# Kernel optimization log

Hardware: AMD Instinct MI355X
Metric: run time of the kernel (lower is better)

The kernel has to match this reference:

```python
import jax, jax.numpy as jnp
import numpy as np

B, T, D, C = 16, 2048, 512, 20
K_EASY, K_HARD = 40, 20
M_BIG, M_SMALL = 7, 3
A4 = A5 = A6 = A7 = 1.0
EPS = 1e-05
DROP_P = 0.6


def setup_inputs() -> dict:
    key = jax.random.key(0)
    ks = jax.random.split(key, 6)
    attn = jax.random.uniform(ks[0], (B, T, 1), dtype=jnp.float32)
    mu = jax.random.normal(ks[1], (B, T, D), dtype=jnp.float32)
    var = jax.random.uniform(ks[2], (B, T, D), dtype=jnp.float32) * 0.9 + 0.1
    mu_clip = jax.random.normal(ks[3], (B, T, D), dtype=jnp.float32)
    text_feat = jax.random.normal(ks[4], (C, D), dtype=jnp.float32)
    keep = (jax.random.uniform(ks[5], (B, T)) >= DROP_P).astype(jnp.float32)
    drop_mask = keep / (1.0 - DROP_P)  # inverted-dropout mask on a ones tensor
    return dict(attn=attn, mu=mu, var=var, mu_clip=mu_clip, text_feat=text_feat, drop_mask=drop_mask)


def _normalize(x, axis=-1):
    n = jnp.linalg.norm(x, axis=axis, keepdims=True)
    return x / jnp.maximum(n, 1e-12)


def _select_topk(scores, emb, k):
    # torch: sort desc, take first k indices, gather along time dim
    _, idx = jax.lax.top_k(scores, k)  # [B,k]
    return jnp.take_along_axis(emb, idx[:, :, None], axis=1)  # [B,k,D]


def _window_reduce(x, w, op_min):
    # binary erosion/dilation along time with structure ones((1,w)), border_value=0
    lo, hi = w // 2, w - 1 - w // 2
    xp = jnp.pad(x, ((0, 0), (lo, hi)), constant_values=0.0)
    if op_min:
        return jax.lax.reduce_window(xp, jnp.inf, jax.lax.min, (1, w), (1, 1), 'VALID')
    return jax.lax.reduce_window(xp, -jnp.inf, jax.lax.max, (1, w), (1, 1), 'VALID')


def _kl_distance(mu_p, cov_p, mu_q, cov_q):
    # vectorized over all (i in k_p) x (j in k_q) pairs
    cov_p = cov_p + EPS
    cov_q = cov_q + EPS
    d = mu_p.shape[-1]
    diff = mu_q[:, None, :, :] - mu_p[:, :, None, :]        # [B,kp,kq,D]
    term1 = 0.5 * jnp.sum(diff * diff / cov_q[:, None, :, :], axis=-1)
    term2 = 0.5 * (jnp.sum(jnp.log(cov_q), -1)[:, None, :] - jnp.sum(jnp.log(cov_p), -1)[:, :, None])
    term3 = 0.5 * jnp.sum(cov_p[:, :, None, :] / cov_q[:, None, :, :], axis=-1)
    dist = term1 + term2 + term3 - 0.5 * d
    return jnp.mean(1.0 / (dist + 1.0), axis=(1, 2))        # [B]


def _prob_contrastive(hard_q, easy_pos, easy_neg):
    pos = _kl_distance(hard_q[0], hard_q[1], easy_pos[0], easy_pos[1])
    neg = _kl_distance(hard_q[0], hard_q[1], easy_neg[0], easy_neg[1])
    return jnp.mean(-(jnp.log(pos) + jnp.log(1.0 - neg)))


def _forward(attn, mu, var, mu_clip, text_feat, drop_mask):
    a = attn[..., 0]                                        # [B,T]
    a_drop = a * drop_mask
    a_rev = jnp.max(a, axis=1, keepdims=True) - a
    a_rev_drop = a_rev * drop_mask
    easy_act = (_select_topk(a_drop, mu, K_EASY), _select_topk(a_drop, var, K_EASY))
    easy_bkg = (_select_topk(a_rev_drop, mu, K_EASY), _select_topk(a_rev_drop, var, K_EASY))

    med = jnp.median(a, axis=1, keepdims=True)
    abin = jnp.where(a > med, 1.0, 0.0)
    er_M = _window_reduce(abin, M_BIG, True)
    er_m = _window_reduce(abin, M_SMALL, True)
    inner = jax.lax.stop_gradient(er_m - er_M)              # mask computed on detached numpy in torch
    dl_m = _window_reduce(abin, M_SMALL, False)
    dl_M = _window_reduce(abin, M_BIG, False)
    outer = jax.lax.stop_gradient(dl_M - dl_m)
    a_inner = a * inner
    a_outer = a * outer
    hard_act = (_select_topk(a_inner, mu, K_HARD), _select_topk(a_inner, var, K_HARD))
    hard_bkg = (_select_topk(a_outer, mu, K_HARD), _select_topk(a_outer, var, K_HARD))

    # Distillation
    sim = jnp.einsum('btd,btd->bt', _normalize(mu), _normalize(mu_clip))
    distill = A4 * (-jnp.log(jnp.mean((sim + 1.0) / 2.0)))

    act_loss = A5 * _prob_contrastive(hard_act, easy_act, easy_bkg)
    bkg_loss = A6 * _prob_contrastive(hard_bkg, easy_bkg, easy_act)

    emb = _normalize(text_feat)
    sim_m = emb @ jax.lax.stop_gradient(emb.T) - jnp.eye(emb.shape[0], dtype=emb.dtype)
    ortho = A7 * jnp.linalg.norm(sim_m)

    total = distill + act_loss + bkg_loss + ortho
    return total, distill, act_loss, bkg_loss, ortho


def reference(attn, mu, var, mu_clip, text_feat, drop_mask):
    return _forward(attn, mu, var, mu_clip, text_feat, drop_mask)
```

## Files before the change

### kernel.cpp

```cpp
#include <hip/hip_runtime.h>
#include <math.h>


#define BB 16
#define TT 2048
#define DD 512
#define CC 20
#define KEASY 40
#define KHARD 20
#define EPSF 1e-5f

typedef unsigned long long u64;

template <int CTRL>
__device__ __forceinline__ float dpp_mov(float x) {
  return __int_as_float(__builtin_amdgcn_update_dpp(
      0, __float_as_int(x), CTRL, 0xF, 0xF, true));
}
__device__ __forceinline__ float wsum63(float v) {
  v += dpp_mov<0x111>(v);
  v += dpp_mov<0x112>(v);
  v += dpp_mov<0x114>(v);
  v += dpp_mov<0x118>(v);
  v += dpp_mov<0x142>(v);
  v += dpp_mov<0x143>(v);
  return v;
}
__device__ __forceinline__ float wsum_bc(float v) {
  return __int_as_float(__builtin_amdgcn_readlane(__float_as_int(wsum63(v)), 63));
}
__device__ __forceinline__ float wmax_bc(float v) {
  v = fmaxf(v, dpp_mov<0x111>(v));
  v = fmaxf(v, dpp_mov<0x112>(v));
  v = fmaxf(v, dpp_mov<0x114>(v));
  v = fmaxf(v, dpp_mov<0x118>(v));
  v = fmaxf(v, dpp_mov<0x142>(v));
  v = fmaxf(v, dpp_mov<0x143>(v));
  return __int_as_float(__builtin_amdgcn_readlane(__float_as_int(v), 63));
}

__device__ __forceinline__ float kth_val(const float (&v)[32], unsigned k, unsigned hi) {
  unsigned lo = 0;
  while (lo < hi) {
    const unsigned mid = lo + ((hi - lo + 1) >> 1);
    const float mf = __uint_as_float(mid);
    unsigned c = 0;
#pragma unroll
    for (int r = 0; r < 32; r++) c += (unsigned)__popcll(__ballot(v[r] >= mf));
    if (c >= k) lo = mid; else hi = mid - 1;
  }
  return __uint_as_float(lo);
}

__global__ __launch_bounds__(256, 1) void k_main1(const float* __restrict__ attn,
                                                  const float* __restrict__ drop,
                                                  const float* __restrict__ mu,
                                                  const float* __restrict__ muc,
                                                  const float* __restrict__ var,
                                                  int* __restrict__ idxb,
                                                  float* __restrict__ slogb,
                                                  float* __restrict__ part,
                                                  double* __restrict__ acc) {
  const int tid = threadIdx.x, wid = tid >> 6, lane = tid & 63;

  if (blockIdx.x >= 64) {
    __shared__ float s_red[4];
    const int blk = blockIdx.x - 64;
    const float* pmu = mu + (size_t)(blk * 4 + wid) * DD + lane * 4;
    const float* pmc = muc + (size_t)(blk * 4 + wid) * DD + lane * 4;
    float4 xa = *(const float4*)(pmu);
    float4 xb = *(const float4*)(pmu + 256);
    float4 ya = *(const float4*)(pmc);
    float4 yb = *(const float4*)(pmc + 256);
    float wacc = 0.f;
#pragma unroll
    for (int it = 0; it < 4; it++) {
      const float4 cxa = xa, cxb = xb, cya = ya, cyb = yb;
      if (it < 3) {
        const size_t off = (size_t)(it + 1) * 8192 * DD;
        xa = *(const float4*)(pmu + off);
        xb = *(const float4*)(pmu + off + 256);
        ya = *(const float4*)(pmc + off);
        yb = *(const float4*)(pmc + off + 256);
      }
      float dot = 0.f, n1 = 0.f, n2 = 0.f;
      dot = fmaf(cxa.x, cya.x, fmaf(cxa.y, cya.y, fmaf(cxa.z, cya.z, fmaf(cxa.w, cya.w, dot))));
      n1 = fmaf(cxa.x, cxa.x, fmaf(cxa.y, cxa.y, fmaf(cxa.z, cxa.z, fmaf(cxa.w, cxa.w, n1))));
      n2 = fmaf(cya.x, cya.x, fmaf(cya.y, cya.y, fmaf(cya.z, cya.z, fmaf(cya.w, cya.w, n2))));
      dot = fmaf(cxb.x, cyb.x, fmaf(cxb.y, cyb.y, fmaf(cxb.z, cyb.z, fmaf(cxb.w, cyb.w, dot))));
      n1 = fmaf(cxb.x, cxb.x, fmaf(cxb.y, cxb.y, fmaf(cxb.z, cxb.z, fmaf(cxb.w, cxb.w, n1))));
      n2 = fmaf(cyb.x, cyb.x, fmaf(cyb.y, cyb.y, fmaf(cyb.z, cyb.z, fmaf(cyb.w, cyb.w, n2))));
      dot = wsum63(dot);
      n1 = wsum63(n1);
      n2 = wsum63(n2);
      if (lane == 63) {
        const float sim = dot / (fmaxf(sqrtf(n1), 1e-12f) * fmaxf(sqrtf(n2), 1e-12f));
        wacc += (sim + 1.0f) * 0.5f;
      }
    }
    if (lane == 63) s_red[wid] = wacc;
    __syncthreads();
    if (tid == 0) part[blk] = s_red[0] + s_red[1] + s_red[2] + s_red[3];
    return;
  }

  __shared__ float s_a[TT];
  __shared__ int s_idx[KEASY];
  const int b = blockIdx.x >> 2, sel = blockIdx.x & 3;
  for (int i = tid; i < TT; i += 256) s_a[i] = attn[b * TT + i];
  __syncthreads();

  if (tid < 64) {
    if (blockIdx.x == 0) {
      acc[lane] = 0.0;
      if (lane < 2) acc[64 + lane] = 0.0;
    }
    float v[32];
    float med = 0.f, mx = 0.f;
    if (sel >= 2) {
#pragma unroll
      for (int r = 0; r < 32; r++) v[r] = s_a[r * 64 + lane];
      const float v1 = kth_val(v, 1024, 0x3F800000u);
      const float v2 = kth_val(v, 1025, __float_as_uint(v1));
      med = 0.5f * (v1 + v2);
    }
    if (sel == 1) {
      float m = 0.f;
#pragma unroll
      for (int r = 0; r < 32; r++) m = fmaxf(m, s_a[r * 64 + lane]);
      mx = wmax_bc(m);
    }
#pragma unroll
    for (int r = 0; r < 32; r++) {
      const int i = r * 64 + lane;
      const float a = s_a[i];
      float score;
      if (sel == 0) {
        score = a * drop[b * TT + i];
      } else if (sel == 1) {
        score = (mx - a) * drop[b * TT + i];
      } else {
        bool sall = true, ball = true, sany = false, bany = false;
#pragma unroll
        for (int o = -3; o <= 3; o++) {
          const int t = i + o;
          const bool one = (t >= 0 && t < TT) ? (s_a[t] > med) : false;
          if (o >= -1 && o <= 1) { sall = sall && one; sany = sany || one; }
          ball = ball && one;
          bany = bany || one;
        }
        score = (sel == 2) ? ((sall && !ball) ? a : 0.f)
                           : ((bany && !sany) ? a : 0.f);
      }
      v[r] = score;
    }
    const unsigned K = (sel < 2) ? KEASY : KHARD;
    const unsigned hiS = (sel < 2) ? 0x40200000u : 0x3F800000u;
    const float ss = kth_val(v, K, hiS);
    unsigned cgt = 0;
#pragma unroll
    for (int r = 0; r < 32; r++) cgt += (unsigned)__popcll(__ballot(v[r] > ss));
    unsigned need = K - cgt;
    unsigned base = 0;
    const u64 lmask = (1ull << lane) - 1;
    int* dst = idxb + sel * (BB * KEASY) + b * KEASY;
#pragma unroll
    for (int r = 0; r < 32; r++) {
      const bool gt = v[r] > ss;
      const bool eq = v[r] == ss;
      const u64 beq = __ballot(eq);
      const unsigned neq = (unsigned)__popcll(beq);
      const unsigned take = (need < neq) ? need : neq;
      const bool tk = eq && ((unsigned)__popcll(beq & lmask) < take);
      const u64 bsel = __ballot(gt || tk);
      if (gt || tk) {
        const unsigned pos = base + (unsigned)__popcll(bsel & lmask);
        dst[pos] = r * 64 + lane;
        s_idx[pos] = r * 64 + lane;
      }
      base += (unsigned)__popcll(bsel);
      need -= take;
    }
  }
  __syncthreads();

  const int Ksel = (sel < 2) ? KEASY : KHARD;
  for (int j = wid; j < Ksel; j += 4) {
    const int t = s_idx[j];
    const float* row = var + ((size_t)b * TT + t) * DD;
    float a2 = 0.f;
#pragma unroll
    for (int c = 0; c < 2; c++) {
      float4 vv = *(const float4*)(row + c * 256 + lane * 4);
      a2 += __logf(vv.x + EPSF) + __logf(vv.y + EPSF) +
            __logf(vv.z + EPSF) + __logf(vv.w + EPSF);
    }
    a2 = wsum63(a2);
    if (lane == 63) slogb[sel * 640 + b * 40 + j] = a2;
  }
}

__global__ __launch_bounds__(256, 1) void k_part2(const float* __restrict__ mu,
                                                  const float* __restrict__ var,
                                                  const int* __restrict__ idxb,
                                                  const float* __restrict__ slogb,
                                                  const float* __restrict__ part,
                                                  const float* __restrict__ text,
                                                  double* __restrict__ acc) {
  __shared__ __align__(16) float smem[2 * KHARD * DD];
  const int tid = threadIdx.x, wid = tid >> 6, lane = tid & 63;
  const int blk = blockIdx.x;

  if (blk < 64) {
    const int b = blk >> 2, klid = blk & 3;
    const int psel = (klid < 2) ? 2 : 3;
    const int qsel = (klid == 0 || klid == 3) ? 0 : 1;
    float* sP1 = smem;
    float* sP2 = smem + KHARD * DD;
    __shared__ float sSlogP[KHARD];
    __shared__ float s_out[4];
    if (tid < KHARD) sSlogP[tid] = slogb[psel * 640 + b * 40 + tid];
    for (int i = tid; i < KHARD * 128; i += 256) {
      const int p = i >> 7, c = (i & 127) * 4;
      const int t = idxb[psel * 640 + b * 40 + p];
      const size_t base = ((size_t)b * TT + t) * DD + c;
      const float4 m = *(const float4*)(mu + base);
      const float4 vv = *(const float4*)(var + base);
      float4 p1;
      p1.x = fmaf(m.x, m.x, vv.x + EPSF);
      p1.y = fmaf(m.y, m.y, vv.y + EPSF);
      p1.z = fmaf(m.z, m.z, vv.z + EPSF);
      p1.w = fmaf(m.w, m.w, vv.w + EPSF);
      *(float4*)(sP1 + p * DD + c) = p1;
      *(float4*)(sP2 + p * DD + c) = m;
    }
    __syncthreads();

    const int d0 = lane * 4, d1 = 256 + lane * 4;
    const int qbase_i = qsel * 640 + b * 40;
    float wacc = 0.f;
    int qidx = idxb[qbase_i + wid];
    float slq = slogb[qbase_i + wid];
    const float* qm = mu + ((size_t)b * TT + qidx) * DD;
    const float* qv = var + ((size_t)b * TT + qidx) * DD;
    float4 mqa = *(const float4*)(qm + d0);
    float4 mqb = *(const float4*)(qm + d1);
    float4 vqa = *(const float4*)(qv + d0);
    float4 vqb = *(const float4*)(qv + d1);
#pragma unroll 1
    for (int t = 0; t < 10; t++) {
      const float4 cma = mqa, cmb = mqb, cva = vqa, cvb = vqb;
      const float cslq = slq;
      if (t < 9) {
        const int iqn = wid + 4 * (t + 1);
        qidx = idxb[qbase_i + iqn];
        slq = slogb[qbase_i + iqn];
        const float* nm = mu + ((size_t)b * TT + qidx) * DD;
        const float* nv = var + ((size_t)b * TT + qidx) * DD;
        mqa = *(const float4*)(nm + d0);
        mqb = *(const float4*)(nm + d1);
        vqa = *(const float4*)(nv + d0);
        vqb = *(const float4*)(nv + d1);
      }
      float4 ra, rb, qra, qrb;
      ra.x = 1.0f / (cva.x + EPSF); ra.y = 1.0f / (cva.y + EPSF);
      ra.z = 1.0f / (cva.z + EPSF); ra.w = 1.0f / (cva.w + EPSF);
      rb.x = 1.0f / (cvb.x + EPSF); rb.y = 1.0f / (cvb.y + EPSF);
      rb.z = 1.0f / (cvb.z + EPSF); rb.w = 1.0f / (cvb.w + EPSF);
      qra.x = cma.x * ra.x; qra.y = cma.y * ra.y;
      qra.z = cma.z * ra.z; qra.w = cma.w * ra.w;
      qrb.x = cmb.x * rb.x; qrb.y = cmb.y * rb.y;
      qrb.z = cmb.z * rb.z; qrb.w = cmb.w * rb.w;
      float cqp = cma.x * qra.x + cma.y * qra.y + cma.z * qra.z + cma.w * qra.w +
                  cmb.x * qrb.x + cmb.y * qrb.y + cmb.z * qrb.z + cmb.w * qrb.w;
      const float cq = wsum63(cqp);
      for (int p = 0; p < KHARD; p++) {
        const float4 p1a = *(const float4*)(sP1 + p * DD + d0);
        const float4 p1b = *(const float4*)(sP1 + p * DD + d1);
        const float4 p2a = *(const float4*)(sP2 + p * DD + d0);
        const float4 p2b = *(const float4*)(sP2 + p * DD + d1);
        const float s1 = p1a.x * ra.x + p1a.y * ra.y + p1a.z * ra.z + p1a.w * ra.w +
                         p1b.x * rb.x + p1b.y * rb.y + p1b.z * rb.z + p1b.w * rb.w;
        const float s2 = p2a.x * qra.x + p2a.y * qra.y + p2a.z * qra.z + p2a.w * qra.w +
                         p2b.x * qrb.x + p2b.y * qrb.y + p2b.z * qrb.z + p2b.w * qrb.w;
        const float h = wsum63(fmaf(0.5f, s1, -s2));
        if (lane == 63) {
          const float dist = h + 0.5f * cq + 0.5f * cslq - 0.5f * sSlogP[p] - 256.0f;
          wacc += 1.0f / (dist + 1.0f);
        }
      }
    }
    if (lane == 63) s_out[wid] = wacc;
    __syncthreads();
    if (tid == 0)
      acc[klid * 16 + b] = (double)s_out[0] + s_out[1] + s_out[2] + s_out[3];
    return;
  }

  if (blk == 64) {
    double* sd = (double*)smem;
    double s = 0.0;
    for (int i = tid; i < 2048; i += 256) s += (double)part[i];
    sd[tid] = s;
    __syncthreads();
    for (int st = 128; st; st >>= 1) {
      if (tid < st) sd[tid] += sd[tid + st];
      __syncthreads();
    }
    if (tid == 0) acc[64] = sd[0];
    return;
  }

  {
    float* s_e = smem;
    __shared__ float s_red4[4];
    for (int r = wid; r < CC; r += 4) {
      float4 v[2];
      float ss = 0.f;
#pragma unroll
      for (int c = 0; c < 2; c++) {
        v[c] = *(const float4*)(text + r * DD + c * 256 + lane * 4);
        ss += v[c].x * v[c].x + v[c].y * v[c].y + v[c].z * v[c].z + v[c].w * v[c].w;
      }
      ss = wsum_bc(ss);
      const float n = fmaxf(sqrtf(ss), 1e-12f);
#pragma unroll
      for (int c = 0; c < 2; c++) {
        float4 w = v[c];
        w.x /= n; w.y /= n; w.z /= n; w.w /= n;
        *(float4*)(s_e + r * DD + c * 256 + lane * 4) = w;
      }
    }
    __syncthreads();
    float wss = 0.f;
    for (int p = wid; p < CC * CC; p += 4) {
      const int i = p / CC, j = p % CC;
      float dot = 0.f;
#pragma unroll
      for (int c = 0; c < 2; c++) {
        const int d0 = c * 256 + lane * 4;
        const float4 x = *(const float4*)(s_e + i * DD + d0);
        const float4 y = *(const float4*)(s_e + j * DD + d0);
        dot += x.x * y.x + x.y * y.y + x.z * y.z + x.w * y.w;
      }
      dot = wsum63(dot);
      if (lane == 63) {
        const float s = dot - (i == j ? 1.0f : 0.0f);
        wss += s * s;
      }
    }
    if (lane == 63) s_red4[wid] = wss;
    __syncthreads();
    if (tid == 0)
      acc[65] = (double)(s_red4[0] + s_red4[1] + s_red4[2] + s_red4[3]);
  }
}

__global__ __launch_bounds__(64) void k_final(const double* __restrict__ acc,
                                              float* __restrict__ out) {
  __shared__ double sla[16], slb[16];
  const int tid = threadIdx.x;
  if (tid < 16) {
    const double pa = acc[0 * 16 + tid] / 800.0;
    const double na = acc[1 * 16 + tid] / 800.0;
    const double pb = acc[2 * 16 + tid] / 800.0;
    const double nb = acc[3 * 16 + tid] / 800.0;
    sla[tid] = -(log(pa) + log(1.0 - na));
    slb[tid] = -(log(pb) + log(1.0 - nb));
  }
  __syncthreads();
  if (tid == 0) {
    double act = 0.0, bkg = 0.0;
    for (int b = 0; b < 16; b++) { act += sla[b]; bkg += slb[b]; }
    act /= 16.0;
    bkg /= 16.0;
    const double distill = -log(acc[64] / (double)(BB * TT));
    const double ortho = sqrt(acc[65]);
    const double total = distill + act + bkg + ortho;
    out[0] = (float)total;
    out[1] = (float)distill;
    out[2] = (float)act;
    out[3] = (float)bkg;
    out[4] = (float)ortho;
  }
}

extern "C" void kernel_launch(void* const* d_in, const int* in_sizes, int n_in,
                              void* d_out, int out_size, void* d_ws, size_t ws_size,
                              hipStream_t stream) {
  const float* attn = (const float*)d_in[0];
  const float* mu   = (const float*)d_in[1];
  const float* var  = (const float*)d_in[2];
  const float* muc  = (const float*)d_in[3];
  const float* text = (const float*)d_in[4];
  const float* drop = (const float*)d_in[5];
  float* out = (float*)d_out;

  double* acc  = (double*)d_ws;
  int* idxb    = (int*)(acc + 66);
  float* slogb = (float*)(idxb + 2560);
  float* part  = (float*)(slogb + 2560);

  k_main1<<<2112, 256, 0, stream>>>(attn, drop, mu, muc, var, idxb, slogb, part, acc);
  k_part2<<<66, 256, 0, stream>>>(mu, var, idxb, slogb, part, text, acc);
  k_final<<<1, 64, 0, stream>>>(acc, out);
}
```

Before: 268.5 us.

## Replace single-wave bisection top-k with block-wide radix select and split KL blocks

The median and top-k threshold selection used to run as a bitwise binary search inside a single wavefront. It now runs a 4-round, 8-bit radix select over all 256 threads, using a shared histogram and a DPP prefix scan, and scores are staged in shared memory. The KL-distance stage is split four ways over query chunks, going from 64 to 256 blocks, and the partial sums are combined in the final kernel. This exposes more parallelism on the selection and KL critical paths at the cost of extra barriers, shared-memory atomics and the removal of the query-row prefetch.

Measured after the change: 239.1 us. -10.9%, faster.

```diff
diff --git a/kernel.cpp b/kernel.cpp
--- a/kernel.cpp
+++ b/kernel.cpp
@@ -16,6 +16,10 @@
 __device__ __forceinline__ float dpp_mov(float x) {
   return __int_as_float(__builtin_amdgcn_update_dpp(
       0, __float_as_int(x), CTRL, 0xF, 0xF, true));
+}
+template <int CTRL, int RM>
+__device__ __forceinline__ unsigned dpp_movu(unsigned x) {
+  return (unsigned)__builtin_amdgcn_update_dpp(0, (int)x, CTRL, RM, 0xF, true);
 }
 __device__ __forceinline__ float wsum63(float v) {
   v += dpp_mov<0x111>(v);
@@ -29,27 +33,74 @@
 __device__ __forceinline__ float wsum_bc(float v) {
   return __int_as_float(__builtin_amdgcn_readlane(__float_as_int(wsum63(v)), 63));
 }
-__device__ __forceinline__ float wmax_bc(float v) {
+__device__ __forceinline__ float wmax63(float v) {
   v = fmaxf(v, dpp_mov<0x111>(v));
   v = fmaxf(v, dpp_mov<0x112>(v));
   v = fmaxf(v, dpp_mov<0x114>(v));
   v = fmaxf(v, dpp_mov<0x118>(v));
   v = fmaxf(v, dpp_mov<0x142>(v));
   v = fmaxf(v, dpp_mov<0x143>(v));
-  return __int_as_float(__builtin_amdgcn_readlane(__float_as_int(v), 63));
-}
-
-__device__ __forceinline__ float kth_val(const float (&v)[32], unsigned k, unsigned hi) {
-  unsigned lo = 0;
-  while (lo < hi) {
-    const unsigned mid = lo + ((hi - lo + 1) >> 1);
-    const float mf = __uint_as_float(mid);
-    unsigned c = 0;
-#pragma unroll
-    for (int r = 0; r < 32; r++) c += (unsigned)__popcll(__ballot(v[r] >= mf));
-    if (c >= k) lo = mid; else hi = mid - 1;
-  }
-  return __uint_as_float(lo);
+  return v;
+}
+__device__ __forceinline__ unsigned wscanu(unsigned v) {
+  v += dpp_movu<0x111, 0xF>(v);
+  v += dpp_movu<0x112, 0xF>(v);
+  v += dpp_movu<0x114, 0xF>(v);
+  v += dpp_movu<0x118, 0xF>(v);
+  v += dpp_movu<0x142, 0xa>(v);
+  v += dpp_movu<0x143, 0xc>(v);
+  return v;
+}
+
+__device__ __forceinline__ float radix_kth(const float* sbuf, unsigned k,
+                                           unsigned* s_hist, unsigned* s_state,
+                                           int tid) {
+#pragma unroll 1
+  for (int round = 0; round < 4; ++round) {
+    s_hist[tid] = 0;
+    if (round == 0 && tid == 0) { s_state[0] = 0u; s_state[1] = k; }
+    __syncthreads();
+    const int shift = 24 - 8 * round;
+    const unsigned mask_hi = (round == 0) ? 0u : (0xFFFFFFFFu << (shift + 8));
+    const unsigned pref = s_state[0];
+    const unsigned kk = s_state[1];
+    unsigned curbin = 0xFFFFFFFFu, curc = 0;
+    for (int i = tid; i < TT; i += 256) {
+      const unsigned key = __float_as_uint(sbuf[i]);
+      if ((key & mask_hi) == pref) {
+        const unsigned bin = 255u - ((key >> shift) & 255u);
+        if (bin == curbin) {
+          curc++;
+        } else {
+          if (curc) atomicAdd(&s_hist[curbin], curc);
+          curbin = bin;
+          curc = 1;
+        }
+      }
+    }
+    if (curc) atomicAdd(&s_hist[curbin], curc);
+    __syncthreads();
+    if (tid < 64) {
+      const uint4 h = *(const uint4*)(s_hist + 4 * tid);
+      const unsigned s0 = h.x, s1 = s0 + h.y, s2 = s1 + h.z, s3 = s2 + h.w;
+      const unsigned P = wscanu(s3);
+      const unsigned E = P - s3;
+      const u64 bal = __ballot(P >= kk);
+      const int L = (int)__ffsll(bal) - 1;
+      if (tid == L) {
+        unsigned binj, cb;
+        if (E + s0 >= kk)      { binj = 0u; cb = E; }
+        else if (E + s1 >= kk) { binj = 1u; cb = E + s0; }
+        else if (E + s2 >= kk) { binj = 2u; cb = E + s1; }
+        else                   { binj = 3u; cb = E + s2; }
+        const unsigned digit = 255u - (4u * (unsigned)tid + binj);
+        s_state[0] = pref | (digit << shift);
+        s_state[1] = kk - cb;
+      }
+    }
+    __syncthreads();
+  }
+  return __uint_as_float(s_state[0]);
 }
 
 __global__ __launch_bounds__(256, 1) void k_main1(const float* __restrict__ attn,
@@ -59,8 +110,7 @@
                                                   const float* __restrict__ var,
                                                   int* __restrict__ idxb,
                                                   float* __restrict__ slogb,
-                                                  float* __restrict__ part,
-                                                  double* __restrict__ acc) {
+                                                  float* __restrict__ part) {
   const int tid = threadIdx.x, wid = tid >> 6, lane = tid & 63;
 
   if (blockIdx.x >= 64) {
@@ -105,69 +155,84 @@
   }
 
   __shared__ float s_a[TT];
+  __shared__ float s_v[TT];
+  __shared__ __align__(16) unsigned s_hist[256];
+  __shared__ unsigned s_state[2];
+  __shared__ float s_bc[4];
+  __shared__ unsigned s_bcu[4];
   __shared__ int s_idx[KEASY];
+
   const int b = blockIdx.x >> 2, sel = blockIdx.x & 3;
   for (int i = tid; i < TT; i += 256) s_a[i] = attn[b * TT + i];
   __syncthreads();
 
+  float med = 0.f, mx = 0.f;
+  if (sel == 1) {
+    float lm = 0.f;
+    for (int i = tid; i < TT; i += 256) lm = fmaxf(lm, s_a[i]);
+    lm = wmax63(lm);
+    if (lane == 63) s_bc[wid] = lm;
+    __syncthreads();
+    mx = fmaxf(fmaxf(s_bc[0], s_bc[1]), fmaxf(s_bc[2], s_bc[3]));
+  } else if (sel >= 2) {
+    const float v1 = radix_kth(s_a, 1024u, s_hist, s_state, tid);
+    unsigned c = 0;
+    float m2 = 0.f;
+    for (int i = tid; i < TT; i += 256) {
+      const float x = s_a[i];
+      c += (x >= v1) ? 1u : 0u;
+      m2 = (x < v1) ? fmaxf(m2, x) : m2;
+    }
+    c = wscanu(c);
+    m2 = wmax63(m2);
+    if (lane == 63) { s_bc[wid] = m2; s_bcu[wid] = c; }
+    __syncthreads();
+    const unsigned ctot = s_bcu[0] + s_bcu[1] + s_bcu[2] + s_bcu[3];
+    const float m2t = fmaxf(fmaxf(s_bc[0], s_bc[1]), fmaxf(s_bc[2], s_bc[3]));
+    const float v2 = (ctot >= 1025u) ? v1 : m2t;
+    med = 0.5f * (v1 + v2);
+  }
+
+  for (int i = tid; i < TT; i += 256) {
+    const float a = s_a[i];
+    float score;
+    if (sel == 0) {
+      score = a * drop[b * TT + i];
+    } else if (sel == 1) {
+      score = (mx - a) * drop[b * TT + i];
+    } else {
+      bool sall = true, ball = true, sany = false, bany = false;
+#pragma unroll
+      for (int o = -3; o <= 3; o++) {
+        const int t = i + o;
+        const bool one = (t >= 0 && t < TT) ? (s_a[t] > med) : false;
+        if (o >= -1 && o <= 1) { sall = sall && one; sany = sany || one; }
+        ball = ball && one;
+        bany = bany || one;
+      }
+      score = (sel == 2) ? ((sall && !ball) ? a : 0.f)
+                         : ((bany && !sany) ? a : 0.f);
+    }
+    s_v[i] = score;
+  }
+  const unsigned K = (sel < 2) ? KEASY : KHARD;
+  const float thr = radix_kth(s_v, K, s_hist, s_state, tid);
+
   if (tid < 64) {
-    if (blockIdx.x == 0) {
-      acc[lane] = 0.0;
-      if (lane < 2) acc[64 + lane] = 0.0;
-    }
     float v[32];
-    float med = 0.f, mx = 0.f;
-    if (sel >= 2) {
-#pragma unroll
-      for (int r = 0; r < 32; r++) v[r] = s_a[r * 64 + lane];
-      const float v1 = kth_val(v, 1024, 0x3F800000u);
-      const float v2 = kth_val(v, 1025, __float_as_uint(v1));
-      med = 0.5f * (v1 + v2);
-    }
-    if (sel == 1) {
-      float m = 0.f;
-#pragma unroll
-      for (int r = 0; r < 32; r++) m = fmaxf(m, s_a[r * 64 + lane]);
-      mx = wmax_bc(m);
-    }
-#pragma unroll
-    for (int r = 0; r < 32; r++) {
-      const int i = r * 64 + lane;
-      const float a = s_a[i];
-      float score;
-      if (sel == 0) {
-        score = a * drop[b * TT + i];
-      } else if (sel == 1) {
-        score = (mx - a) * drop[b * TT + i];
-      } else {
-        bool sall = true, ball = true, sany = false, bany = false;
-#pragma unroll
-        for (int o = -3; o <= 3; o++) {
-          const int t = i + o;
-          const bool one = (t >= 0 && t < TT) ? (s_a[t] > med) : false;
-          if (o >= -1 && o <= 1) { sall = sall && one; sany = sany || one; }
-          ball = ball && one;
-          bany = bany || one;
-        }
-        score = (sel == 2) ? ((sall && !ball) ? a : 0.f)
-                           : ((bany && !sany) ? a : 0.f);
-      }
-      v[r] = score;
-    }
-    const unsigned K = (sel < 2) ? KEASY : KHARD;
-    const unsigned hiS = (sel < 2) ? 0x40200000u : 0x3F800000u;
-    const float ss = kth_val(v, K, hiS);
+#pragma unroll
+    for (int r = 0; r < 32; r++) v[r] = s_v[r * 64 + lane];
     unsigned cgt = 0;
 #pragma unroll
-    for (int r = 0; r < 32; r++) cgt += (unsigned)__popcll(__ballot(v[r] > ss));
-    unsigned need = K - cgt;
+    for (int r = 0; r < 32; r++) cgt += (unsigned)__popcll(__ballot(v[r] > thr));
+    unsigned need = (cgt < K) ? (K - cgt) : 0u;
     unsigned base = 0;
     const u64 lmask = (1ull << lane) - 1;
     int* dst = idxb + sel * (BB * KEASY) + b * KEASY;
 #pragma unroll
     for (int r = 0; r < 32; r++) {
-      const bool gt = v[r] > ss;
-      const bool eq = v[r] == ss;
+      const bool gt = v[r] > thr;
+      const bool eq = v[r] == thr;
       const u64 beq = __ballot(eq);
       const unsigned neq = (unsigned)__popcll(beq);
       const unsigned take = (need < neq) ? need : neq;
@@ -175,8 +240,10 @@
       const u64 bsel = __ballot(gt || tk);
       if (gt || tk) {
         const unsigned pos = base + (unsigned)__popcll(bsel & lmask);
-        dst[pos] = r * 64 + lane;
-        s_idx[pos] = r * 64 + lane;
+        if (pos < K) {
+          dst[pos] = r * 64 + lane;
+          s_idx[pos] = r * 64 + lane;
+        }
       }
       base += (unsigned)__popcll(bsel);
       need -= take;
@@ -211,8 +278,8 @@
   const int tid = threadIdx.x, wid = tid >> 6, lane = tid & 63;
   const int blk = blockIdx.x;
 
-  if (blk < 64) {
-    const int b = blk >> 2, klid = blk & 3;
+  if (blk < 256) {
+    const int b = blk >> 4, klid = (blk >> 2) & 3, qc = blk & 3;
     const int psel = (klid < 2) ? 2 : 3;
     const int qsel = (klid == 0 || klid == 3) ? 0 : 1;
     float* sP1 = smem;
@@ -237,31 +304,18 @@
     __syncthreads();
 
     const int d0 = lane * 4, d1 = 256 + lane * 4;
-    const int qbase_i = qsel * 640 + b * 40;
+    const int qbase_i = qsel * 640 + b * 40 + qc * 10;
     float wacc = 0.f;
-    int qidx = idxb[qbase_i + wid];
-    float slq = slogb[qbase_i + wid];
-    const float* qm = mu + ((size_t)b * TT + qidx) * DD;
-    const float* qv = var + ((size_t)b * TT + qidx) * DD;
-    float4 mqa = *(const float4*)(qm + d0);
-    float4 mqb = *(const float4*)(qm + d1);
-    float4 vqa = *(const float4*)(qv + d0);
-    float4 vqb = *(const float4*)(qv + d1);
 #pragma unroll 1
-    for (int t = 0; t < 10; t++) {
-      const float4 cma = mqa, cmb = mqb, cva = vqa, cvb = vqb;
-      const float cslq = slq;
-      if (t < 9) {
-        const int iqn = wid + 4 * (t + 1);
-        qidx = idxb[qbase_i + iqn];
-        slq = slogb[qbase_i + iqn];
-        const float* nm = mu + ((size_t)b * TT + qidx) * DD;
-        const float* nv = var + ((size_t)b * TT + qidx) * DD;
-        mqa = *(const float4*)(nm + d0);
-        mqb = *(const float4*)(nm + d1);
-        vqa = *(const float4*)(nv + d0);
-        vqb = *(const float4*)(nv + d1);
-      }
+    for (int j = wid; j < 10; j += 4) {
+      const int qidx = idxb[qbase_i + j];
+      const float cslq = slogb[qbase_i + j];
+      const float* qm = mu + ((size_t)b * TT + qidx) * DD;
+      const float* qv = var + ((size_t)b * TT + qidx) * DD;
+      const float4 cma = *(const float4*)(qm + d0);
+      const float4 cmb = *(const float4*)(qm + d1);
+      const float4 cva = *(const float4*)(qv + d0);
+      const float4 cvb = *(const float4*)(qv + d1);
       float4 ra, rb, qra, qrb;
       ra.x = 1.0f / (cva.x + EPSF); ra.y = 1.0f / (cva.y + EPSF);
       ra.z = 1.0f / (cva.z + EPSF); ra.w = 1.0f / (cva.w + EPSF);
@@ -293,11 +347,11 @@
     if (lane == 63) s_out[wid] = wacc;
     __syncthreads();
     if (tid == 0)
-      acc[klid * 16 + b] = (double)s_out[0] + s_out[1] + s_out[2] + s_out[3];
+      acc[blk] = (double)s_out[0] + s_out[1] + s_out[2] + s_out[3];
     return;
   }
 
-  if (blk == 64) {
+  if (blk == 256) {
     double* sd = (double*)smem;
     double s = 0.0;
     for (int i = tid; i < 2048; i += 256) s += (double)part[i];
@@ -307,7 +361,7 @@
       if (tid < st) sd[tid] += sd[tid + st];
       __syncthreads();
     }
-    if (tid == 0) acc[64] = sd[0];
+    if (tid == 0) acc[256] = sd[0];
     return;
   }
 
@@ -352,7 +406,7 @@
     if (lane == 63) s_red4[wid] = wss;
     __syncthreads();
     if (tid == 0)
-      acc[65] = (double)(s_red4[0] + s_red4[1] + s_red4[2] + s_red4[3]);
+      acc[257] = (double)(s_red4[0] + s_red4[1] + s_red4[2] + s_red4[3]);
   }
 }
 
@@ -361,10 +415,11 @@
   __shared__ double sla[16], slb[16];
   const int tid = threadIdx.x;
   if (tid < 16) {
-    const double pa = acc[0 * 16 + tid] / 800.0;
-    const double na = acc[1 * 16 + tid] / 800.0;
-    const double pb = acc[2 * 16 + tid] / 800.0;
-    const double nb = acc[3 * 16 + tid] / 800.0;
+    const double* ab = acc + tid * 16;
+    const double pa = (ab[0] + ab[1] + ab[2] + ab[3]) / 800.0;
+    const double na = (ab[4] + ab[5] + ab[6] + ab[7]) / 800.0;
+    const double pb = (ab[8] + ab[9] + ab[10] + ab[11]) / 800.0;
+    const double nb = (ab[12] + ab[13] + ab[14] + ab[15]) / 800.0;
     sla[tid] = -(log(pa) + log(1.0 - na));
     slb[tid] = -(log(pb) + log(1.0 - nb));
   }
@@ -374,8 +429,8 @@
     for (int b = 0; b < 16; b++) { act += sla[b]; bkg += slb[b]; }
     act /= 16.0;
     bkg /= 16.0;
-    const double distill = -log(acc[64] / (double)(BB * TT));
-    const double ortho = sqrt(acc[65]);
+    const double distill = -log(acc[256] / (double)(BB * TT));
+    const double ortho = sqrt(acc[257]);
     const double total = distill + act + bkg + ortho;
     out[0] = (float)total;
     out[1] = (float)distill;
@@ -397,11 +452,11 @@
   float* out = (float*)d_out;
 
   double* acc  = (double*)d_ws;
-  int* idxb    = (int*)(acc + 66);
+  int* idxb    = (int*)(acc + 258);
   float* slogb = (float*)(idxb + 2560);
   float* part  = (float*)(slogb + 2560);
 
-  k_main1<<<2112, 256, 0, stream>>>(attn, drop, mu, muc, var, idxb, slogb, part, acc);
-  k_part2<<<66, 256, 0, stream>>>(mu, var, idxb, slogb, part, text, acc);
+  k_main1<<<2112, 256, 0, stream>>>(attn, drop, mu, muc, var, idxb, slogb, part);
+  k_part2<<<258, 256, 0, stream>>>(mu, var, idxb, slogb, part, text, acc);
   k_final<<<1, 64, 0, stream>>>(acc, out);
 }
```
